# Kernel optimization log

Hardware: AMD Instinct MI355X
Metric: run time of the kernel (lower is better)

Reference implementation:

```python
import jax, jax.numpy as jnp
import numpy as np

B, T, F, H, E = 32, 512, 64, 64, 32  # batch, time, features(=sequence_length), hidden_dim, encoding_size


def setup_inputs() -> dict:
    key = jax.random.key(0)
    ks = jax.random.split(key, 14)
    sc = 0.05
    return {
        "x": jax.random.normal(ks[0], (B, T, F), jnp.float32),
        "s": jax.random.normal(ks[1], (B, T, E), jnp.float32),
        # gating FFN params
        "ffn_w1": jax.random.normal(ks[2], (F, H), jnp.float32) * sc,
        "ffn_b1": jnp.zeros((H,), jnp.float32),
        "ffn_w2": jax.random.normal(ks[3], (E, H), jnp.float32) * sc,
        "ffn_b2": jnp.zeros((H,), jnp.float32),
        "ffn_w3": jax.random.normal(ks[4], (H, F), jnp.float32) * sc,
        "ffn_b3": jnp.zeros((F,), jnp.float32),
        # per-feature expert FFN_j params (F experts, each Dense(1->H), ELU, Dense(H->H))
        "exp_w1": jax.random.normal(ks[5], (F, H), jnp.float32) * sc,  # weight of Dense(1->H) per feature
        "exp_b1": jnp.zeros((F, H), jnp.float32),
        "exp_w3": jax.random.normal(ks[6], (F, H, H), jnp.float32) * sc,
        "exp_b3": jnp.zeros((F, H), jnp.float32),
    }


def reference(x, s, ffn_w1, ffn_b1, ffn_w2, ffn_b2, ffn_w3, ffn_b3,
              exp_w1, exp_b1, exp_w3, exp_b3):
    # gating network: softmax over feature axis
    g = jnp.einsum('btf,fh->bth', x, ffn_w1) + ffn_b1 \
        + jnp.einsum('bte,eh->bth', s, ffn_w2) + ffn_b2
    logits = jnp.einsum('bth,hf->btf', jax.nn.elu(g), ffn_w3) + ffn_b3
    w_t = jax.nn.softmax(logits, axis=2)  # [B,T,F]

    # per-feature experts, batched: Dense(1->H) is a rank-1 outer product
    h = jax.nn.elu(x[..., None] * exp_w1[None, None] + exp_b1[None, None])  # [B,T,F,H]
    expert_out = jnp.einsum('btfh,fhk->btfk', h, exp_w3) + exp_b3[None, None]  # [B,T,F,H]

    # gate-weighted sum over features
    return jnp.einsum('btfk,btf->btk', expert_out, w_t)  # [B,T,H]
```

## Files before the change

### kernel.cpp

```cpp
#include <hip/hip_runtime.h>
#include <hip/hip_bf16.h>
#include <math.h>

#define NTOK 16384

typedef __attribute__((ext_vector_type(8))) short short8;
typedef __attribute__((ext_vector_type(4))) float f32x4;

__device__ __forceinline__ unsigned short bf16_rne(float x) {
    unsigned int u = __float_as_uint(x);
    u += 0x7fffu + ((u >> 16) & 1u);
    return (unsigned short)(u >> 16);
}
__device__ __forceinline__ unsigned pack_bf16(float a, float b) {
    union { __hip_bfloat162 h; unsigned u; } cv;
    cv.h = __float22bfloat162_rn(make_float2(a, b));
    return cv.u;
}
__device__ __forceinline__ float eluf(float z) {
    return z > 0.0f ? z : (__expf(z) - 1.0f);
}

__global__ __launch_bounds__(256)
void prepass(const float* __restrict__ ew3, const float* __restrict__ eb3,
             unsigned short* __restrict__ ws) {
    __shared__ float tile[64 * 65];
    const int bid = blockIdx.x, tid = threadIdx.x;
    const float* src = (bid < 64) ? (ew3 + (size_t)bid * 4096) : eb3;

    const int r = tid >> 2, c0 = (tid & 3) * 16;
    #pragma unroll
    for (int j = 0; j < 4; ++j) {
        float4 v = *(const float4*)(src + r * 64 + c0 + j * 4);
        tile[r * 65 + c0 + j * 4 + 0] = v.x;
        tile[r * 65 + c0 + j * 4 + 1] = v.y;
        tile[r * 65 + c0 + j * 4 + 2] = v.z;
        tile[r * 65 + c0 + j * 4 + 3] = v.w;
    }
    __syncthreads();

    uint4* dst = (uint4*)(ws + (size_t)bid * 4096);
    #pragma unroll
    for (int it = 0; it < 2; ++it) {
        const int idx = tid + it * 256;
        const int c = idx >> 8, u = (idx >> 6) & 3, l = idx & 63;
        const int m = l & 15, q = (l >> 4) & 3;
        const int rb = c * 32 + q * 8, col = u * 16 + m;
        unsigned pw[4];
        #pragma unroll
        for (int p = 0; p < 4; ++p) {
            unsigned lo = bf16_rne(tile[(rb + 2 * p    ) * 65 + col]);
            unsigned hi = bf16_rne(tile[(rb + 2 * p + 1) * 65 + col]);
            pw[p] = lo | (hi << 16);
        }
        uint4 pk; pk.x = pw[0]; pk.y = pw[1]; pk.z = pw[2]; pk.w = pw[3];
        dst[idx] = pk;
    }
}

__global__ __launch_bounds__(256, 4)
void moe_fused(const float* __restrict__ x,   const float* __restrict__ s,
               const float* __restrict__ fw1, const float* __restrict__ fb1,
               const float* __restrict__ fw2, const float* __restrict__ fb2,
               const float* __restrict__ fw3, const float* __restrict__ fb3,
               const float* __restrict__ ew1, const float* __restrict__ eb1,
               const float* __restrict__ ew3, const float* __restrict__ eb3,
               const unsigned short* __restrict__ w3img, int use_ws,
               float* __restrict__ out)
{
    __shared__ float wts[16 * 65];
    __shared__ __align__(16) float ped[4][16 * 68];

    const int tid = threadIdx.x;
    const int wv = tid >> 6, lane = tid & 63;
    const int tokbase = blockIdx.x * 16;

    {
        const int t0w = wv * 4;
        const float* xw = x + (size_t)(tokbase + t0w) * 64;
        const float* sw = s + (size_t)(tokbase + t0w) * 32;
        float g[4];
        const float b0 = fb1[lane] + fb2[lane];
        #pragma unroll
        for (int t = 0; t < 4; ++t) g[t] = b0;
        for (int f = 0; f < 64; ++f) {
            const float w = fw1[f * 64 + lane];
            #pragma unroll
            for (int t = 0; t < 4; ++t) g[t] = fmaf(xw[t * 64 + f], w, g[t]);
        }
        for (int e = 0; e < 32; ++e) {
            const float w = fw2[e * 64 + lane];
            #pragma unroll
            for (int t = 0; t < 4; ++t) g[t] = fmaf(sw[t * 32 + e], w, g[t]);
        }
        #pragma unroll
        for (int t = 0; t < 4; ++t) g[t] = eluf(g[t]);

        float lg[4];
        const float b3 = fb3[lane];
        #pragma unroll
        for (int t = 0; t < 4; ++t) lg[t] = b3;
        for (int h = 0; h < 64; ++h) {
            const float w = fw3[h * 64 + lane];
            #pragma unroll
            for (int t = 0; t < 4; ++t) {
                const float ev = __int_as_float(
                    __builtin_amdgcn_readlane(__float_as_int(g[t]), h));
                lg[t] = fmaf(ev, w, lg[t]);
            }
        }
        #pragma unroll
        for (int t = 0; t < 4; ++t) {
            float mx = lg[t];
            #pragma unroll
            for (int off = 32; off > 0; off >>= 1) mx = fmaxf(mx, __shfl_xor(mx, off));
            const float p = __expf(lg[t] - mx);
            float sm = p;
            #pragma unroll
            for (int off = 32; off > 0; off >>= 1) sm += __shfl_xor(sm, off);
            wts[(t0w + t) * 65 + lane] = p / sm;
        }
    }
    __syncthreads();

    const int m = tid & 15, quad = (tid >> 4) & 3;
    const int f0 = wv * 16;
    f32x4 acc[4];
    #pragma unroll
    for (int u = 0; u < 4; ++u) acc[u] = (f32x4){0.f, 0.f, 0.f, 0.f};

    const float* xcol = x + (size_t)(tokbase + m) * 64;

    for (int ff = 0; ff < 16; ++ff) {
        const int f = f0 + ff;

        short8 b[2][4];
        if (use_ws) {
            const uint4* bp = (const uint4*)(w3img + (size_t)f * 4096);
            #pragma unroll
            for (int c = 0; c < 2; ++c)
                #pragma unroll
                for (int u = 0; u < 4; ++u) {
                    uint4 v = bp[c * 256 + u * 64 + lane];
                    b[c][u] = *(short8*)&v;
                }
        } else {
            #pragma unroll
            for (int c = 0; c < 2; ++c)
                #pragma unroll
                for (int u = 0; u < 4; ++u) {
                    const float* wp = ew3 + (size_t)f * 4096
                                    + (size_t)(c * 32 + quad * 8) * 64 + u * 16 + m;
                    unsigned pw[4];
                    #pragma unroll
                    for (int p = 0; p < 4; ++p)
                        pw[p] = pack_bf16(wp[(2 * p) * 64], wp[(2 * p + 1) * 64]);
                    uint4 v; v.x = pw[0]; v.y = pw[1]; v.z = pw[2]; v.w = pw[3];
                    b[c][u] = *(short8*)&v;
                }
        }

        const float xv = xcol[f];
        const float wt = wts[m * 65 + f];
        short8 a[2];
        #pragma unroll
        for (int c = 0; c < 2; ++c) {
            const float* w1p = ew1 + f * 64 + c * 32 + quad * 8;
            const float* b1p = eb1 + f * 64 + c * 32 + quad * 8;
            const float4 w1a = *(const float4*)(w1p);
            const float4 w1b = *(const float4*)(w1p + 4);
            const float4 b1a = *(const float4*)(b1p);
            const float4 b1b = *(const float4*)(b1p + 4);
            float v0 = wt * eluf(fmaf(xv, w1a.x, b1a.x));
            float v1 = wt * eluf(fmaf(xv, w1a.y, b1a.y));
            float v2 = wt * eluf(fmaf(xv, w1a.z, b1a.z));
            float v3 = wt * eluf(fmaf(xv, w1a.w, b1a.w));
            float v4 = wt * eluf(fmaf(xv, w1b.x, b1b.x));
            float v5 = wt * eluf(fmaf(xv, w1b.y, b1b.y));
            float v6 = wt * eluf(fmaf(xv, w1b.z, b1b.z));
            float v7 = wt * eluf(fmaf(xv, w1b.w, b1b.w));
            uint4 av;
            av.x = pack_bf16(v0, v1); av.y = pack_bf16(v2, v3);
            av.z = pack_bf16(v4, v5); av.w = pack_bf16(v6, v7);
            a[c] = *(short8*)&av;
        }

        #pragma unroll
        for (int u = 0; u < 4; ++u) {
            acc[u] = __builtin_amdgcn_mfma_f32_16x16x32_bf16(a[0], b[0][u], acc[u], 0, 0, 0);
            acc[u] = __builtin_amdgcn_mfma_f32_16x16x32_bf16(a[1], b[1][u], acc[u], 0, 0, 0);
        }
    }

    if (wv < 2) {
        const int e0 = wv * 32 + quad * 8;
        float v[8];
        #pragma unroll
        for (int j = 0; j < 8; ++j) v[j] = wts[m * 65 + e0 + j];
        uint4 av;
        av.x = pack_bf16(v[0], v[1]); av.y = pack_bf16(v[2], v[3]);
        av.z = pack_bf16(v[4], v[5]); av.w = pack_bf16(v[6], v[7]);
        short8 a = *(short8*)&av;

        short8 b[4];
        if (use_ws) {
            const uint4* bp = (const uint4*)(w3img + (size_t)64 * 4096);
            #pragma unroll
            for (int u = 0; u < 4; ++u) {
                uint4 bv = bp[wv * 256 + u * 64 + lane];
                b[u] = *(short8*)&bv;
            }
        } else {
            #pragma unroll
            for (int u = 0; u < 4; ++u) {
                const float* wp = eb3 + (size_t)e0 * 64 + u * 16 + m;
                unsigned pw[4];
                #pragma unroll
                for (int p = 0; p < 4; ++p)
                    pw[p] = pack_bf16(wp[(2 * p) * 64], wp[(2 * p + 1) * 64]);
                uint4 bv; bv.x = pw[0]; bv.y = pw[1]; bv.z = pw[2]; bv.w = pw[3];
                b[u] = *(short8*)&bv;
            }
        }
        #pragma unroll
        for (int u = 0; u < 4; ++u)
            acc[u] = __builtin_amdgcn_mfma_f32_16x16x32_bf16(a, b[u], acc[u], 0, 0, 0);
    }

    #pragma unroll
    for (int u = 0; u < 4; ++u)
        #pragma unroll
        for (int r = 0; r < 4; ++r)
            ped[wv][(quad * 4 + r) * 68 + u * 16 + m] = acc[u][r];
    __syncthreads();

    const int t = tid >> 4, kq = tid & 15;
    const float4 p0 = *(const float4*)&ped[0][t * 68 + kq * 4];
    const float4 p1 = *(const float4*)&ped[1][t * 68 + kq * 4];
    const float4 p2 = *(const float4*)&ped[2][t * 68 + kq * 4];
    const float4 p3 = *(const float4*)&ped[3][t * 68 + kq * 4];
    float4 o;
    o.x = (p0.x + p1.x) + (p2.x + p3.x);
    o.y = (p0.y + p1.y) + (p2.y + p3.y);
    o.z = (p0.z + p1.z) + (p2.z + p3.z);
    o.w = (p0.w + p1.w) + (p2.w + p3.w);
    *(float4*)(out + (size_t)(tokbase + t) * 64 + kq * 4) = o;
}

extern "C" void kernel_launch(void* const* d_in, const int* in_sizes, int n_in,
                              void* d_out, int out_size, void* d_ws, size_t ws_size,
                              hipStream_t stream) {
    const float* x   = (const float*)d_in[0];
    const float* s   = (const float*)d_in[1];
    const float* fw1 = (const float*)d_in[2];
    const float* fb1 = (const float*)d_in[3];
    const float* fw2 = (const float*)d_in[4];
    const float* fb2 = (const float*)d_in[5];
    const float* fw3 = (const float*)d_in[6];
    const float* fb3 = (const float*)d_in[7];
    const float* ew1 = (const float*)d_in[8];
    const float* eb1 = (const float*)d_in[9];
    const float* ew3 = (const float*)d_in[10];
    const float* eb3 = (const float*)d_in[11];
    float* out = (float*)d_out;

    const size_t ws_need = (size_t)65 * 4096 * sizeof(unsigned short);
    const int use_ws = (ws_size >= ws_need) && (((uintptr_t)d_ws & 15) == 0);
    unsigned short* w3img = (unsigned short*)d_ws;

    if (use_ws) prepass<<<dim3(65), dim3(256), 0, stream>>>(ew3, eb3, w3img);
    moe_fused<<<dim3(NTOK / 16), dim3(256), 0, stream>>>(x, s, fw1, fb1, fw2, fb2,
                                                         fw3, fb3, ew1, eb1, ew3, eb3,
                                                         w3img, use_ws, out);
}
```

Baseline: 134.5 us.

## Merge weight-repack prepass into main kernel with flag-based producer/consumer sync

Replaces the two launches with one grid. The first 65 blocks repack the expert weights into the bf16 MFMA layout and publish per-block release flags. Consumer blocks spin on those flags with a bounded wait and fall back to converting fp32 weights directly if the wait runs out. It also stages x in LDS, computes the gating logits from an LDS copy of the ELU activations instead of per-element readlanes, and prefetches the next feature's B fragments and x and gate values one iteration ahead. The flags are never reset, so later calls may see flags still set from an earlier call and read the image before this call's producers rewrite it. That is only safe while the weights stay the same. Spinning consumers can also hold CUs that producers need.

Result: slower. 152.8 us (+13.6%).

```diff
diff --git a/kernel.cpp b/kernel.cpp
--- a/kernel.cpp
+++ b/kernel.cpp
@@ -3,6 +3,8 @@
 #include <math.h>
 
 #define NTOK 16384
+#define PROD 65
+#define CONS (NTOK / 16)
 
 typedef __attribute__((ext_vector_type(8))) short short8;
 typedef __attribute__((ext_vector_type(4))) float f32x4;
@@ -13,71 +15,119 @@
     return (unsigned short)(u >> 16);
 }
 __device__ __forceinline__ unsigned pack_bf16(float a, float b) {
-    union { __hip_bfloat162 h; unsigned u; } cv;
-    cv.h = __float22bfloat162_rn(make_float2(a, b));
-    return cv.u;
+    return (unsigned)bf16_rne(a) | ((unsigned)bf16_rne(b) << 16);
 }
 __device__ __forceinline__ float eluf(float z) {
     return z > 0.0f ? z : (__expf(z) - 1.0f);
 }
 
-__global__ __launch_bounds__(256)
-void prepass(const float* __restrict__ ew3, const float* __restrict__ eb3,
-             unsigned short* __restrict__ ws) {
-    __shared__ float tile[64 * 65];
-    const int bid = blockIdx.x, tid = threadIdx.x;
-    const float* src = (bid < 64) ? (ew3 + (size_t)bid * 4096) : eb3;
-
-    const int r = tid >> 2, c0 = (tid & 3) * 16;
+__device__ __forceinline__ void gen_a(const float* __restrict__ ew1,
+                                      const float* __restrict__ eb1,
+                                      int f, int quad, float xv, float wt,
+                                      short8* a) {
     #pragma unroll
-    for (int j = 0; j < 4; ++j) {
-        float4 v = *(const float4*)(src + r * 64 + c0 + j * 4);
-        tile[r * 65 + c0 + j * 4 + 0] = v.x;
-        tile[r * 65 + c0 + j * 4 + 1] = v.y;
-        tile[r * 65 + c0 + j * 4 + 2] = v.z;
-        tile[r * 65 + c0 + j * 4 + 3] = v.w;
+    for (int c = 0; c < 2; ++c) {
+        const float* w1p = ew1 + f * 64 + c * 32 + quad * 8;
+        const float* b1p = eb1 + f * 64 + c * 32 + quad * 8;
+        const float4 w1a = *(const float4*)w1p, w1b = *(const float4*)(w1p + 4);
+        const float4 b1a = *(const float4*)b1p, b1b = *(const float4*)(b1p + 4);
+        uint4 av;
+        av.x = pack_bf16(wt * eluf(fmaf(xv, w1a.x, b1a.x)),
+                         wt * eluf(fmaf(xv, w1a.y, b1a.y)));
+        av.y = pack_bf16(wt * eluf(fmaf(xv, w1a.z, b1a.z)),
+                         wt * eluf(fmaf(xv, w1a.w, b1a.w)));
+        av.z = pack_bf16(wt * eluf(fmaf(xv, w1b.x, b1b.x)),
+                         wt * eluf(fmaf(xv, w1b.y, b1b.y)));
+        av.w = pack_bf16(wt * eluf(fmaf(xv, w1b.z, b1b.z)),
+                         wt * eluf(fmaf(xv, w1b.w, b1b.w)));
+        a[c] = *(short8*)&av;
+    }
+}
+
+__device__ __forceinline__ void gen_b_fp32(const float* __restrict__ w3f,
+                                           int quad, int m, short8 b[2][4]) {
+    #pragma unroll
+    for (int c = 0; c < 2; ++c)
+        #pragma unroll
+        for (int u = 0; u < 4; ++u) {
+            const float* wp = w3f + (size_t)(c * 32 + quad * 8) * 64 + u * 16 + m;
+            uint4 v;
+            v.x = pack_bf16(wp[0],   wp[64]);
+            v.y = pack_bf16(wp[128], wp[192]);
+            v.z = pack_bf16(wp[256], wp[320]);
+            v.w = pack_bf16(wp[384], wp[448]);
+            b[c][u] = *(short8*)&v;
+        }
+}
+
+__global__ __launch_bounds__(256, 4)
+void moe_one(const float* __restrict__ x,   const float* __restrict__ s,
+             const float* __restrict__ fw1, const float* __restrict__ fb1,
+             const float* __restrict__ fw2, const float* __restrict__ fb2,
+             const float* __restrict__ fw3, const float* __restrict__ fb3,
+             const float* __restrict__ ew1, const float* __restrict__ eb1,
+             const float* __restrict__ ew3, const float* __restrict__ eb3,
+             unsigned short* __restrict__ w3img, int use_ws,
+             float* __restrict__ out)
+{
+    __shared__ __align__(16) char smem[30016];
+    const int tid = threadIdx.x;
+    const int bid = blockIdx.x;
+    int* flags = (int*)(w3img + (size_t)PROD * 4096);
+
+    if (bid < PROD) {
+        if (!use_ws) return;
+        float* tile = (float*)smem;
+        const float* src = (bid < 64) ? (ew3 + (size_t)bid * 4096) : eb3;
+        const int r = tid >> 2, c0 = (tid & 3) * 16;
+        #pragma unroll
+        for (int j = 0; j < 4; ++j) {
+            float4 v = *(const float4*)(src + r * 64 + c0 + j * 4);
+            tile[r * 65 + c0 + j * 4 + 0] = v.x;
+            tile[r * 65 + c0 + j * 4 + 1] = v.y;
+            tile[r * 65 + c0 + j * 4 + 2] = v.z;
+            tile[r * 65 + c0 + j * 4 + 3] = v.w;
+        }
+        __syncthreads();
+        uint4* dst = (uint4*)(w3img + (size_t)bid * 4096);
+        #pragma unroll
+        for (int it = 0; it < 2; ++it) {
+            const int idx = tid + it * 256;
+            const int c = idx >> 8, u = (idx >> 6) & 3, l = idx & 63;
+            const int m = l & 15, q = (l >> 4) & 3;
+            const int rb = c * 32 + q * 8, col = u * 16 + m;
+            unsigned pw[4];
+            #pragma unroll
+            for (int p = 0; p < 4; ++p)
+                pw[p] = pack_bf16(tile[(rb + 2 * p) * 65 + col],
+                                  tile[(rb + 2 * p + 1) * 65 + col]);
+            uint4 pk; pk.x = pw[0]; pk.y = pw[1]; pk.z = pw[2]; pk.w = pw[3];
+            dst[idx] = pk;
+        }
+        __syncthreads();
+        if (tid == 0)
+            __hip_atomic_store(&flags[bid], 1, __ATOMIC_RELEASE,
+                               __HIP_MEMORY_SCOPE_AGENT);
+        return;
+    }
+
+    float* xls = (float*)smem;
+    float* wts = (float*)(smem + 4352);
+    float* egs = (float*)(smem + 8512);
+    float* ped = (float*)(smem + 12608);
+
+    const int wv = tid >> 6, lane = tid & 63;
+    const int tokbase = (bid - PROD) * 16;
+
+    {
+        const int t = tid >> 4, fq = (tid & 15) * 4;
+        float4 v = *(const float4*)(x + (size_t)(tokbase + t) * 64 + fq);
+        *(float4*)&xls[t * 68 + fq] = v;
     }
     __syncthreads();
-
-    uint4* dst = (uint4*)(ws + (size_t)bid * 4096);
-    #pragma unroll
-    for (int it = 0; it < 2; ++it) {
-        const int idx = tid + it * 256;
-        const int c = idx >> 8, u = (idx >> 6) & 3, l = idx & 63;
-        const int m = l & 15, q = (l >> 4) & 3;
-        const int rb = c * 32 + q * 8, col = u * 16 + m;
-        unsigned pw[4];
-        #pragma unroll
-        for (int p = 0; p < 4; ++p) {
-            unsigned lo = bf16_rne(tile[(rb + 2 * p    ) * 65 + col]);
-            unsigned hi = bf16_rne(tile[(rb + 2 * p + 1) * 65 + col]);
-            pw[p] = lo | (hi << 16);
-        }
-        uint4 pk; pk.x = pw[0]; pk.y = pw[1]; pk.z = pw[2]; pk.w = pw[3];
-        dst[idx] = pk;
-    }
-}
-
-__global__ __launch_bounds__(256, 4)
-void moe_fused(const float* __restrict__ x,   const float* __restrict__ s,
-               const float* __restrict__ fw1, const float* __restrict__ fb1,
-               const float* __restrict__ fw2, const float* __restrict__ fb2,
-               const float* __restrict__ fw3, const float* __restrict__ fb3,
-               const float* __restrict__ ew1, const float* __restrict__ eb1,
-               const float* __restrict__ ew3, const float* __restrict__ eb3,
-               const unsigned short* __restrict__ w3img, int use_ws,
-               float* __restrict__ out)
-{
-    __shared__ float wts[16 * 65];
-    __shared__ __align__(16) float ped[4][16 * 68];
-
-    const int tid = threadIdx.x;
-    const int wv = tid >> 6, lane = tid & 63;
-    const int tokbase = blockIdx.x * 16;
 
     {
         const int t0w = wv * 4;
-        const float* xw = x + (size_t)(tokbase + t0w) * 64;
         const float* sw = s + (size_t)(tokbase + t0w) * 32;
         float g[4];
         const float b0 = fb1[lane] + fb2[lane];
@@ -86,7 +136,8 @@
         for (int f = 0; f < 64; ++f) {
             const float w = fw1[f * 64 + lane];
             #pragma unroll
-            for (int t = 0; t < 4; ++t) g[t] = fmaf(xw[t * 64 + f], w, g[t]);
+            for (int t = 0; t < 4; ++t)
+                g[t] = fmaf(xls[(t0w + t) * 68 + f], w, g[t]);
         }
         for (int e = 0; e < 32; ++e) {
             const float w = fw2[e * 64 + lane];
@@ -94,20 +145,25 @@
             for (int t = 0; t < 4; ++t) g[t] = fmaf(sw[t * 32 + e], w, g[t]);
         }
         #pragma unroll
-        for (int t = 0; t < 4; ++t) g[t] = eluf(g[t]);
+        for (int t = 0; t < 4; ++t) egs[wv * 256 + t * 64 + lane] = eluf(g[t]);
 
         float lg[4];
         const float b3 = fb3[lane];
         #pragma unroll
         for (int t = 0; t < 4; ++t) lg[t] = b3;
-        for (int h = 0; h < 64; ++h) {
-            const float w = fw3[h * 64 + lane];
-            #pragma unroll
-            for (int t = 0; t < 4; ++t) {
-                const float ev = __int_as_float(
-                    __builtin_amdgcn_readlane(__float_as_int(g[t]), h));
-                lg[t] = fmaf(ev, w, lg[t]);
-            }
+        for (int hq = 0; hq < 16; ++hq) {
+            const float4 e0 = *(const float4*)&egs[wv * 256 + 0 * 64 + hq * 4];
+            const float4 e1 = *(const float4*)&egs[wv * 256 + 1 * 64 + hq * 4];
+            const float4 e2 = *(const float4*)&egs[wv * 256 + 2 * 64 + hq * 4];
+            const float4 e3 = *(const float4*)&egs[wv * 256 + 3 * 64 + hq * 4];
+            const float w0 = fw3[(hq * 4 + 0) * 64 + lane];
+            const float w1 = fw3[(hq * 4 + 1) * 64 + lane];
+            const float w2 = fw3[(hq * 4 + 2) * 64 + lane];
+            const float w3v = fw3[(hq * 4 + 3) * 64 + lane];
+            lg[0] = fmaf(e0.x, w0, fmaf(e0.y, w1, fmaf(e0.z, w2, fmaf(e0.w, w3v, lg[0]))));
+            lg[1] = fmaf(e1.x, w0, fmaf(e1.y, w1, fmaf(e1.z, w2, fmaf(e1.w, w3v, lg[1]))));
+            lg[2] = fmaf(e2.x, w0, fmaf(e2.y, w1, fmaf(e2.z, w2, fmaf(e2.w, w3v, lg[2]))));
+            lg[3] = fmaf(e3.x, w0, fmaf(e3.y, w1, fmaf(e3.z, w2, fmaf(e3.w, w3v, lg[3]))));
         }
         #pragma unroll
         for (int t = 0; t < 4; ++t) {
@@ -125,85 +181,78 @@
 
     const int m = tid & 15, quad = (tid >> 4) & 3;
     const int f0 = wv * 16;
+    bool ok = false;
+    if (use_ws) {
+        const int fidx = (lane < 16) ? (f0 + lane) : 64;
+        for (int spin = 0; spin < 256 && !ok; ++spin) {
+            int v = 1;
+            if (lane <= 16)
+                v = __hip_atomic_load(&flags[fidx], __ATOMIC_RELAXED,
+                                      __HIP_MEMORY_SCOPE_AGENT);
+            ok = (__ballot(v == 1) == ~0ull);
+            if (!ok) __builtin_amdgcn_s_sleep(1);
+        }
+        if (ok) __builtin_amdgcn_fence(__ATOMIC_ACQUIRE, "agent");
+    }
+
     f32x4 acc[4];
     #pragma unroll
     for (int u = 0; u < 4; ++u) acc[u] = (f32x4){0.f, 0.f, 0.f, 0.f};
 
-    const float* xcol = x + (size_t)(tokbase + m) * 64;
-
-    for (int ff = 0; ff < 16; ++ff) {
-        const int f = f0 + ff;
-
-        short8 b[2][4];
-        if (use_ws) {
-            const uint4* bp = (const uint4*)(w3img + (size_t)f * 4096);
-            #pragma unroll
-            for (int c = 0; c < 2; ++c)
+    if (ok) {
+        const uint4* bb = (const uint4*)w3img;
+        uint4 bn[8];
+        #pragma unroll
+        for (int i = 0; i < 8; ++i)
+            bn[i] = bb[(size_t)f0 * 512 + (i >> 2) * 256 + (i & 3) * 64 + lane];
+        float xnv = xls[m * 68 + f0];
+        float wnv = wts[m * 65 + f0];
+        #pragma unroll
+        for (int ff = 0; ff < 16; ++ff) {
+            uint4 bc[8];
+            #pragma unroll
+            for (int i = 0; i < 8; ++i) bc[i] = bn[i];
+            const float xv = xnv, wt = wnv;
+            if (ff < 15) {
                 #pragma unroll
-                for (int u = 0; u < 4; ++u) {
-                    uint4 v = bp[c * 256 + u * 64 + lane];
-                    b[c][u] = *(short8*)&v;
-                }
-        } else {
-            #pragma unroll
-            for (int c = 0; c < 2; ++c)
-                #pragma unroll
-                for (int u = 0; u < 4; ++u) {
-                    const float* wp = ew3 + (size_t)f * 4096
-                                    + (size_t)(c * 32 + quad * 8) * 64 + u * 16 + m;
-                    unsigned pw[4];
-                    #pragma unroll
-                    for (int p = 0; p < 4; ++p)
-                        pw[p] = pack_bf16(wp[(2 * p) * 64], wp[(2 * p + 1) * 64]);
-                    uint4 v; v.x = pw[0]; v.y = pw[1]; v.z = pw[2]; v.w = pw[3];
-                    b[c][u] = *(short8*)&v;
-                }
-        }
-
-        const float xv = xcol[f];
-        const float wt = wts[m * 65 + f];
-        short8 a[2];
-        #pragma unroll
-        for (int c = 0; c < 2; ++c) {
-            const float* w1p = ew1 + f * 64 + c * 32 + quad * 8;
-            const float* b1p = eb1 + f * 64 + c * 32 + quad * 8;
-            const float4 w1a = *(const float4*)(w1p);
-            const float4 w1b = *(const float4*)(w1p + 4);
-            const float4 b1a = *(const float4*)(b1p);
-            const float4 b1b = *(const float4*)(b1p + 4);
-            float v0 = wt * eluf(fmaf(xv, w1a.x, b1a.x));
-            float v1 = wt * eluf(fmaf(xv, w1a.y, b1a.y));
-            float v2 = wt * eluf(fmaf(xv, w1a.z, b1a.z));
-            float v3 = wt * eluf(fmaf(xv, w1a.w, b1a.w));
-            float v4 = wt * eluf(fmaf(xv, w1b.x, b1b.x));
-            float v5 = wt * eluf(fmaf(xv, w1b.y, b1b.y));
-            float v6 = wt * eluf(fmaf(xv, w1b.z, b1b.z));
-            float v7 = wt * eluf(fmaf(xv, w1b.w, b1b.w));
-            uint4 av;
-            av.x = pack_bf16(v0, v1); av.y = pack_bf16(v2, v3);
-            av.z = pack_bf16(v4, v5); av.w = pack_bf16(v6, v7);
-            a[c] = *(short8*)&av;
-        }
-
-        #pragma unroll
-        for (int u = 0; u < 4; ++u) {
-            acc[u] = __builtin_amdgcn_mfma_f32_16x16x32_bf16(a[0], b[0][u], acc[u], 0, 0, 0);
-            acc[u] = __builtin_amdgcn_mfma_f32_16x16x32_bf16(a[1], b[1][u], acc[u], 0, 0, 0);
+                for (int i = 0; i < 8; ++i)
+                    bn[i] = bb[(size_t)(f0 + ff + 1) * 512 + (i >> 2) * 256 + (i & 3) * 64 + lane];
+                xnv = xls[m * 68 + f0 + ff + 1];
+                wnv = wts[m * 65 + f0 + ff + 1];
+            }
+            short8 a[2];
+            gen_a(ew1, eb1, f0 + ff, quad, xv, wt, a);
+            #pragma unroll
+            for (int u = 0; u < 4; ++u) {
+                acc[u] = __builtin_amdgcn_mfma_f32_16x16x32_bf16(a[0], *(short8*)&bc[u],     acc[u], 0, 0, 0);
+                acc[u] = __builtin_amdgcn_mfma_f32_16x16x32_bf16(a[1], *(short8*)&bc[4 + u], acc[u], 0, 0, 0);
+            }
+        }
+    } else {
+        for (int ff = 0; ff < 16; ++ff) {
+            const int f = f0 + ff;
+            short8 b[2][4];
+            gen_b_fp32(ew3 + (size_t)f * 4096, quad, m, b);
+            short8 a[2];
+            gen_a(ew1, eb1, f, quad, xls[m * 68 + f], wts[m * 65 + f], a);
+            #pragma unroll
+            for (int u = 0; u < 4; ++u) {
+                acc[u] = __builtin_amdgcn_mfma_f32_16x16x32_bf16(a[0], b[0][u], acc[u], 0, 0, 0);
+                acc[u] = __builtin_amdgcn_mfma_f32_16x16x32_bf16(a[1], b[1][u], acc[u], 0, 0, 0);
+            }
         }
     }
 
     if (wv < 2) {
         const int e0 = wv * 32 + quad * 8;
-        float v[8];
-        #pragma unroll
-        for (int j = 0; j < 8; ++j) v[j] = wts[m * 65 + e0 + j];
         uint4 av;
-        av.x = pack_bf16(v[0], v[1]); av.y = pack_bf16(v[2], v[3]);
-        av.z = pack_bf16(v[4], v[5]); av.w = pack_bf16(v[6], v[7]);
+        av.x = pack_bf16(wts[m * 65 + e0 + 0], wts[m * 65 + e0 + 1]);
+        av.y = pack_bf16(wts[m * 65 + e0 + 2], wts[m * 65 + e0 + 3]);
+        av.z = pack_bf16(wts[m * 65 + e0 + 4], wts[m * 65 + e0 + 5]);
+        av.w = pack_bf16(wts[m * 65 + e0 + 6], wts[m * 65 + e0 + 7]);
         short8 a = *(short8*)&av;
-
         short8 b[4];
-        if (use_ws) {
+        if (ok) {
             const uint4* bp = (const uint4*)(w3img + (size_t)64 * 4096);
             #pragma unroll
             for (int u = 0; u < 4; ++u) {
@@ -213,12 +262,12 @@
         } else {
             #pragma unroll
             for (int u = 0; u < 4; ++u) {
-                const float* wp = eb3 + (size_t)e0 * 64 + u * 16 + m;
-                unsigned pw[4];
-                #pragma unroll
-                for (int p = 0; p < 4; ++p)
-                    pw[p] = pack_bf16(wp[(2 * p) * 64], wp[(2 * p + 1) * 64]);
-                uint4 bv; bv.x = pw[0]; bv.y = pw[1]; bv.z = pw[2]; bv.w = pw[3];
+                const float* wp = eb3 + (size_t)(wv * 32 + quad * 8) * 64 + u * 16 + m;
+                uint4 bv;
+                bv.x = pack_bf16(wp[0],   wp[64]);
+                bv.y = pack_bf16(wp[128], wp[192]);
+                bv.z = pack_bf16(wp[256], wp[320]);
+                bv.w = pack_bf16(wp[384], wp[448]);
                 b[u] = *(short8*)&bv;
             }
         }
@@ -231,14 +280,14 @@
     for (int u = 0; u < 4; ++u)
         #pragma unroll
         for (int r = 0; r < 4; ++r)
-            ped[wv][(quad * 4 + r) * 68 + u * 16 + m] = acc[u][r];
+            ped[wv * 1088 + (quad * 4 + r) * 68 + u * 16 + m] = acc[u][r];
     __syncthreads();
 
     const int t = tid >> 4, kq = tid & 15;
-    const float4 p0 = *(const float4*)&ped[0][t * 68 + kq * 4];
-    const float4 p1 = *(const float4*)&ped[1][t * 68 + kq * 4];
-    const float4 p2 = *(const float4*)&ped[2][t * 68 + kq * 4];
-    const float4 p3 = *(const float4*)&ped[3][t * 68 + kq * 4];
+    const float4 p0 = *(const float4*)&ped[0 * 1088 + t * 68 + kq * 4];
+    const float4 p1 = *(const float4*)&ped[1 * 1088 + t * 68 + kq * 4];
+    const float4 p2 = *(const float4*)&ped[2 * 1088 + t * 68 + kq * 4];
+    const float4 p3 = *(const float4*)&ped[3 * 1088 + t * 68 + kq * 4];
     float4 o;
     o.x = (p0.x + p1.x) + (p2.x + p3.x);
     o.y = (p0.y + p1.y) + (p2.y + p3.y);
@@ -264,12 +313,11 @@
     const float* eb3 = (const float*)d_in[11];
     float* out = (float*)d_out;
 
-    const size_t ws_need = (size_t)65 * 4096 * sizeof(unsigned short);
+    const size_t ws_need = (size_t)PROD * 4096 * sizeof(unsigned short) + PROD * sizeof(int);
     const int use_ws = (ws_size >= ws_need) && (((uintptr_t)d_ws & 15) == 0);
     unsigned short* w3img = (unsigned short*)d_ws;
 
-    if (use_ws) prepass<<<dim3(65), dim3(256), 0, stream>>>(ew3, eb3, w3img);
-    moe_fused<<<dim3(NTOK / 16), dim3(256), 0, stream>>>(x, s, fw1, fb1, fw2, fb2,
-                                                         fw3, fb3, ew1, eb1, ew3, eb3,
-                                                         w3img, use_ws, out);
-}
+    moe_one<<<dim3(PROD + CONS), dim3(256), 0, stream>>>(
+        x, s, fw1, fb1, fw2, fb2, fw3, fb3, ew1, eb1, ew3, eb3,
+        w3img, use_ws, out);
+}
```
